# Optimization experiments

Measured on AMD Instinct MI355X. Metric: run time of the kernel, lower is better.

## Reference

```python
import jax, jax.numpy as jnp
import numpy as np

H, N, CH = 256, 64, 1

def _r2c(x):
    return x[..., 0] + 1j * x[..., 1]

def setup_inputs() -> dict:
    key = jax.random.key(0)
    kA, kB, kC, kdt = jax.random.split(key, 4)
    # Build a Hurwitz A (skew-Hermitian - 0.5*I) so dA = (I-dt/2 A)^-1 (I+dt/2 A) has spectral radius < 1
    M = jax.random.normal(kA, (H, N, N, 2), dtype=jnp.float32) / np.float32(np.sqrt(N))
    Mc = _r2c(M)
    Ac = 0.5 * (Mc - jnp.conjugate(jnp.swapaxes(Mc, -1, -2))) - 0.5 * jnp.eye(N, dtype=Mc.dtype)
    A = jnp.stack([Ac.real, Ac.imag], axis=-1)  # (H,N,N,2)
    B = jax.random.normal(kB, (H, N, 2), dtype=jnp.float32)
    C = jax.random.normal(kC, (CH, H, N, 2), dtype=jnp.float32)
    # log_dt uniform in [log(1e-3), log(1e-1)], shape (H,1) per bilinear docstring
    log_dt = jax.random.uniform(kdt, (H, 1), dtype=jnp.float32,
                                minval=np.float32(np.log(1e-3)), maxval=np.float32(np.log(1e-1)))
    return {"A": A, "B": B, "C": C, "log_dt": log_dt, "L": 2048}

def _bilinear(dt, Ac, Bc):
    # dt: (H,1), Ac: (H,N,N) complex, Bc: (H,N) complex
    n = Ac.shape[-1]
    I = jnp.eye(n, dtype=Ac.dtype)
    half = (dt.astype(Ac.real.dtype) / 2)[:, None]  # (H,1,1)
    A_back = I - half * Ac
    A_fwd = I + half * Ac
    dB = dt.astype(Ac.dtype) * jnp.linalg.solve(A_back, Bc[..., None])[..., 0]  # (H,N)
    dA = jnp.linalg.solve(A_back, A_fwd)  # (H,N,N)
    return dA, dB

def _krylov(L, dA, dB):
    # x[..., l] = dA^l dB via squaring-doubling, matches S4 krylov math
    x = dB[..., None]  # (H,N,1)
    A_ = dA
    while x.shape[-1] < L:
        x = jnp.concatenate([x, jnp.einsum('hnm,hml->hnl', A_, x)], axis=-1)
        A_ = A_ @ A_
    return x[..., :L]

def reference(A, B, C, log_dt, L):
    Ac, Bc, Cc = _r2c(A), _r2c(B), _r2c(C)
    dt = jnp.exp(log_dt)  # (H,1)
    dA, dB = _bilinear(dt, Ac, Bc)
    x = _krylov(L, dA, dB)  # (H,N,L) complex
    # k[c,h,l] = sum_n C[c,h,n] * (dA^l dB)[h,n]; torch .float() on complex keeps real part
    k = jnp.einsum('chn,hnl->chl', Cc, x).real.astype(jnp.float32)
    return k
```

## Files before the change

### kernel.cpp

```cpp
#include <hip/hip_runtime.h>
#include <math.h>

#define NH   256
#define NN   64
#define LSEQ 2048
#define RS   72
#define PSZ  4608
#define GSZ  2304
#define NTH  1024

typedef __attribute__((ext_vector_type(8))) short short8;
typedef __attribute__((ext_vector_type(4))) float float4_t;
typedef __attribute__((ext_vector_type(16))) float float16_t;
typedef unsigned short u16;

#define MFMA(a,b,c)   __builtin_amdgcn_mfma_f32_16x16x32_bf16((a),(b),(c),0,0,0)
#define MFMA32(a,b,c) __builtin_amdgcn_mfma_f32_32x32x16_bf16((a),(b),(c),0,0,0)
#define PERM_HI 0x07060302u

static __device__ __forceinline__ void split2(float v, unsigned& hb, unsigned& lb) {
    hb = __float_as_uint(v) & 0xffff0000u;
    lb = __float_as_uint(v - __uint_as_float(hb));
}
static __device__ __forceinline__ float ld2(const u16* hp, const u16* lp, int idx) {
    return __uint_as_float((unsigned)hp[idx] << 16)
         + __uint_as_float((unsigned)lp[idx] << 16);
}
static __device__ __forceinline__ short8 neg8(short8 v) {
    union { short8 s; int i[4]; } u; u.s = v;
#pragma unroll
    for (int m = 0; m < 4; ++m) u.i[m] ^= 0x80008000;
    return u.s;
}

static __device__ __forceinline__ void frag_vals(const unsigned* e, short8& hi, short8& lo) {
    unsigned lb[8];
#pragma unroll
    for (int m = 0; m < 8; ++m) {
        unsigned hv = e[m] & 0xffff0000u;
        lb[m] = __float_as_uint(__uint_as_float(e[m]) - __uint_as_float(hv));
    }
    union { short8 s; unsigned u[4]; } H, L;
#pragma unroll
    for (int m = 0; m < 4; ++m) {
        H.u[m] = __builtin_amdgcn_perm(e[2*m+1],  e[2*m],  PERM_HI);
        L.u[m] = __builtin_amdgcn_perm(lb[2*m+1], lb[2*m], PERM_HI);
    }
    hi = H.s; lo = L.s;
}

template<int ASZ, int BSZ, bool IMAG>
static __device__ __forceinline__ void cmm_tile(
    const u16* __restrict__ Ab, const u16* __restrict__ Bb,
    int arow, int bcol, int fq,
    float4_t& accP, float4_t& accN, float4_t& accI1, float4_t& accI2)
{
#pragma unroll
    for (int ks = 0; ks < 2; ++ks) {
        const int k0 = ks*32 + fq*8;
        const u16* ap = Ab + arow*RS + k0;
        const u16* bp = Bb + bcol*RS + k0;
        short8 Arh = *(const short8*)(ap);
        short8 Arl = *(const short8*)(ap + ASZ);
        short8 Aih = *(const short8*)(ap + 2*ASZ);
        short8 Ail = *(const short8*)(ap + 3*ASZ);
        short8 Brh = *(const short8*)(bp);
        short8 Brl = *(const short8*)(bp + BSZ);
        short8 Bih = *(const short8*)(bp + 2*BSZ);
        short8 Bil = *(const short8*)(bp + 3*BSZ);
        accP = MFMA(Arh, Brh, accP); accP = MFMA(Arh, Brl, accP); accP = MFMA(Arl, Brh, accP);
        accN = MFMA(Aih, Bih, accN); accN = MFMA(Aih, Bil, accN); accN = MFMA(Ail, Bih, accN);
        if (IMAG) {
            accI1 = MFMA(Arh, Bih, accI1); accI1 = MFMA(Arh, Bil, accI1); accI1 = MFMA(Arl, Bih, accI1);
            accI2 = MFMA(Aih, Brh, accI2); accI2 = MFMA(Aih, Brl, accI2); accI2 = MFMA(Ail, Brh, accI2);
        }
    }
}

template<int ASZ, int BSZ>
static __device__ __forceinline__ void cmm_pair(
    const u16* __restrict__ Ab, const u16* __restrict__ Bb,
    int arow, int bcol0, int fq,
    float4_t& P0, float4_t& N0, float4_t& I10, float4_t& I20,
    float4_t& P1, float4_t& N1, float4_t& I11, float4_t& I21)
{
#pragma unroll
    for (int ks = 0; ks < 2; ++ks) {
        const int k0 = ks*32 + fq*8;
        const u16* ap = Ab + arow*RS + k0;
        short8 Arh = *(const short8*)(ap);
        short8 Arl = *(const short8*)(ap + ASZ);
        short8 Aih = *(const short8*)(ap + 2*ASZ);
        short8 Ail = *(const short8*)(ap + 3*ASZ);
        {
            const u16* bp0 = Bb + bcol0*RS + k0;
            short8 Brh = *(const short8*)(bp0);
            short8 Brl = *(const short8*)(bp0 + BSZ);
            short8 Bih = *(const short8*)(bp0 + 2*BSZ);
            short8 Bil = *(const short8*)(bp0 + 3*BSZ);
            P0 = MFMA(Arh, Brh, P0); P0 = MFMA(Arh, Brl, P0); P0 = MFMA(Arl, Brh, P0);
            N0 = MFMA(Aih, Bih, N0); N0 = MFMA(Aih, Bil, N0); N0 = MFMA(Ail, Bih, N0);
            I10 = MFMA(Arh, Bih, I10); I10 = MFMA(Arh, Bil, I10); I10 = MFMA(Arl, Bih, I10);
            I20 = MFMA(Aih, Brh, I20); I20 = MFMA(Aih, Brl, I20); I20 = MFMA(Ail, Brh, I20);
        }
        {
            const u16* bp1 = Bb + (bcol0 + 16)*RS + k0;
            short8 Brh = *(const short8*)(bp1);
            short8 Brl = *(const short8*)(bp1 + BSZ);
            short8 Bih = *(const short8*)(bp1 + 2*BSZ);
            short8 Bil = *(const short8*)(bp1 + 3*BSZ);
            P1 = MFMA(Arh, Brh, P1); P1 = MFMA(Arh, Brl, P1); P1 = MFMA(Arl, Brh, P1);
            N1 = MFMA(Aih, Bih, N1); N1 = MFMA(Aih, Bil, N1); N1 = MFMA(Ail, Bih, N1);
            I11 = MFMA(Arh, Bih, I11); I11 = MFMA(Arh, Bil, I11); I11 = MFMA(Arl, Bih, I11);
            I21 = MFMA(Aih, Brh, I21); I21 = MFMA(Aih, Brl, I21); I21 = MFMA(Ail, Brh, I21);
        }
    }
}

template<int ASZ, int BSZ>
static __device__ __forceinline__ void cmm32_tile2(
    const u16* __restrict__ Ab, const u16* __restrict__ Bb,
    int arow, int bcol, int khalf,
    float16_t& R, float16_t& I)
{
#pragma unroll
    for (int ks = 0; ks < 4; ++ks) {
        const int k0 = ks*16 + khalf;
        const u16* ap = Ab + arow*RS + k0;
        const u16* bp = Bb + bcol*RS + k0;
        short8 Arh = *(const short8*)(ap);
        short8 Arl = *(const short8*)(ap + ASZ);
        short8 Aih = *(const short8*)(ap + 2*ASZ);
        short8 Ail = *(const short8*)(ap + 3*ASZ);
        short8 Brh = *(const short8*)(bp);
        short8 Brl = *(const short8*)(bp + BSZ);
        short8 Bih = *(const short8*)(bp + 2*BSZ);
        short8 Bil = *(const short8*)(bp + 3*BSZ);
        short8 nAih = neg8(Aih), nAil = neg8(Ail);
        R = MFMA32(Arh, Brh, R);  I = MFMA32(Arh, Bih, I);
        R = MFMA32(Arh, Brl, R);  I = MFMA32(Arh, Bil, I);
        R = MFMA32(Arl, Brh, R);  I = MFMA32(Arl, Bih, I);
        R = MFMA32(nAih, Bih, R); I = MFMA32(Aih, Brh, I);
        R = MFMA32(nAih, Bil, R); I = MFMA32(Aih, Brl, I);
        R = MFMA32(nAil, Bih, R); I = MFMA32(Ail, Brh, I);
    }
}

static __device__ __forceinline__ void store_P_vals(
    u16* XR, u16* XT, int ti, int bcol, int fq,
    const float* p_r, const float* p_i)
{
    unsigned hR[4], lR[4], hI[4], lI[4];
#pragma unroll
    for (int r = 0; r < 4; ++r) {
        split2(p_r[r], hR[r], lR[r]);
        split2(p_i[r], hI[r], lI[r]);
        int row = ti*16 + fq*4 + r;
        XR[row*RS + bcol]         = (u16)(hR[r] >> 16);
        XR[PSZ + row*RS + bcol]   = (u16)(lR[r] >> 16);
        XR[2*PSZ + row*RS + bcol] = (u16)(hI[r] >> 16);
        XR[3*PSZ + row*RS + bcol] = (u16)(lI[r] >> 16);
    }
    int tb = bcol*RS + ti*16 + fq*4;
    uint2 w;
    w.x = __builtin_amdgcn_perm(hR[1], hR[0], PERM_HI);
    w.y = __builtin_amdgcn_perm(hR[3], hR[2], PERM_HI);
    *(uint2*)&XT[tb] = w;
    w.x = __builtin_amdgcn_perm(lR[1], lR[0], PERM_HI);
    w.y = __builtin_amdgcn_perm(lR[3], lR[2], PERM_HI);
    *(uint2*)&XT[PSZ + tb] = w;
    w.x = __builtin_amdgcn_perm(hI[1], hI[0], PERM_HI);
    w.y = __builtin_amdgcn_perm(hI[3], hI[2], PERM_HI);
    *(uint2*)&XT[2*PSZ + tb] = w;
    w.x = __builtin_amdgcn_perm(lI[1], lI[0], PERM_HI);
    w.y = __builtin_amdgcn_perm(lI[3], lI[2], PERM_HI);
    *(uint2*)&XT[3*PSZ + tb] = w;
}

static __device__ __forceinline__ void store_P_vals32(
    u16* XR, u16* XT, int trow, int tcol, int lane,
    const float16_t& vR, const float16_t& vI)
{
    const int col = tcol + (lane & 31);
    const int hi4 = (lane >> 5) * 4;
#pragma unroll
    for (int q = 0; q < 4; ++q) {
        unsigned hR[4], lR[4], hI[4], lI[4];
#pragma unroll
        for (int rr = 0; rr < 4; ++rr) {
            const int g = 4*q + rr;
            split2(vR[g], hR[rr], lR[rr]);
            split2(vI[g], hI[rr], lI[rr]);
            const int row = trow + rr + 8*q + hi4;
            XR[row*RS + col]         = (u16)(hR[rr] >> 16);
            XR[PSZ + row*RS + col]   = (u16)(lR[rr] >> 16);
            XR[2*PSZ + row*RS + col] = (u16)(hI[rr] >> 16);
            XR[3*PSZ + row*RS + col] = (u16)(lI[rr] >> 16);
        }
        const int tb = col*RS + trow + 8*q + hi4;
        uint2 w;
        w.x = __builtin_amdgcn_perm(hR[1], hR[0], PERM_HI);
        w.y = __builtin_amdgcn_perm(hR[3], hR[2], PERM_HI);
        *(uint2*)&XT[tb] = w;
        w.x = __builtin_amdgcn_perm(lR[1], lR[0], PERM_HI);
        w.y = __builtin_amdgcn_perm(lR[3], lR[2], PERM_HI);
        *(uint2*)&XT[PSZ + tb] = w;
        w.x = __builtin_amdgcn_perm(hI[1], hI[0], PERM_HI);
        w.y = __builtin_amdgcn_perm(hI[3], hI[2], PERM_HI);
        *(uint2*)&XT[2*PSZ + tb] = w;
        w.x = __builtin_amdgcn_perm(lI[1], lI[0], PERM_HI);
        w.y = __builtin_amdgcn_perm(lI[3], lI[2], PERM_HI);
        *(uint2*)&XT[3*PSZ + tb] = w;
    }
}

__global__ __launch_bounds__(NTH, 4) void ssm_kernel(
    const float* __restrict__ Ag,
    const float* __restrict__ Bg,
    const float* __restrict__ Cg,
    const float* __restrict__ LogDt,
    float* __restrict__ outp)
{
    __shared__ __align__(16) unsigned char lds[130048];
    u16* XR = (u16*)(lds);
    u16* XT = (u16*)(lds +  36864);
    u16* XF = (u16*)(lds +  73728);
    u16* Gm = (u16*)(lds + 110592);
    float* bvr = (float*)(lds + 129024);
    float* bvi = (float*)(lds + 129280);
    float* urr = (float*)(lds + 129536);
    float* uri = (float*)(lds + 129792);

    const int t    = threadIdx.x;
    const int lane = t & 63;
    const int wv   = t >> 6;
    const int fm   = lane & 15, fq = lane >> 4;
    const int h    = blockIdx.x;

    const int tip  = wv >> 1, tjp = wv & 1;
    const int parow = tip*16 + fm;
    const int pb0   = tjp*32 + fm;
    const int pb1   = pb0 + 16;

    const int ti2 = (wv >> 1) & 1, tj2 = wv & 1;
    const int arow32 = ti2*32 + (lane & 31);
    const int bcol32 = tj2*32 + (lane & 31);
    const int khalf  = (lane >> 5) * 8;

    const float dt  = expf(LogDt[h]);
    const float hdt = 0.5f * dt;

    const float2* A2 = (const float2*)(Ag + (size_t)h * NN * NN * 2);
    const float4_t z4 = {0.f, 0.f, 0.f, 0.f};

#pragma unroll
    for (int e = 0; e < 4; ++e) {
        int idx = t + e*NTH;
        int i = idx >> 6, j = idx & 63;
        float2 a = A2[idx];
        unsigned hb, lb;
        split2((i == j ? 1.0f : 0.0f) + hdt * a.x, hb, lb);
        XR[i*RS + j]       = (u16)(hb >> 16);
        XR[PSZ + i*RS + j] = (u16)(lb >> 16);
        XT[j*RS + i]       = (u16)(hb >> 16);
        XT[PSZ + j*RS + i] = (u16)(lb >> 16);
        split2(hdt * a.y, hb, lb);
        XR[2*PSZ + i*RS + j] = (u16)(hb >> 16);
        XR[3*PSZ + i*RS + j] = (u16)(lb >> 16);
        XT[2*PSZ + j*RS + i] = (u16)(hb >> 16);
        XT[3*PSZ + j*RS + i] = (u16)(lb >> 16);
    }
    if (t < NN) {
        float2 bv = ((const float2*)Bg)[h*NN + t];
        float2 cv = ((const float2*)Cg)[h*NN + t];
        bvr[t] = bv.x; bvi[t] = bv.y;
        unsigned hb, lb;
        split2(cv.x, hb, lb);
        Gm[t]       = (u16)(hb >> 16);
        Gm[GSZ + t] = (u16)(lb >> 16);
        split2(cv.y, hb, lb);
        Gm[2*GSZ + t] = (u16)(hb >> 16);
        Gm[3*GSZ + t] = (u16)(lb >> 16);
    }
    __syncthreads();

    if (wv < 8) {
        float4_t P0 = z4, N0 = z4, I10 = z4, I20 = z4;
        float4_t P1 = z4, N1 = z4, I11 = z4, I21 = z4;
#pragma unroll
        for (int ks = 0; ks < 2; ++ks) {
            const int k0 = ks*32 + fq*8;
            unsigned vr[8], vi[8];
#pragma unroll
            for (int j = 0; j < 8; ++j) {
                float2 a = A2[parow*NN + k0 + j];
                vr[j] = __float_as_uint((parow == k0 + j ? 1.0f : 0.0f) - hdt * a.x);
                vi[j] = __float_as_uint(-hdt * a.y);
            }
            short8 Arh, Arl, Aih, Ail;
            frag_vals(vr, Arh, Arl);
            frag_vals(vi, Aih, Ail);
#pragma unroll
            for (int p = 0; p < 2; ++p) {
                const u16* bp = XT + (pb0 + p*16)*RS + k0;
                short8 Brh = *(const short8*)(bp);
                short8 Brl = *(const short8*)(bp + PSZ);
                short8 Bih = *(const short8*)(bp + 2*PSZ);
                short8 Bil = *(const short8*)(bp + 3*PSZ);
                float4_t &aP = p ? P1 : P0, &aN = p ? N1 : N0;
                float4_t &aI1 = p ? I11 : I10, &aI2 = p ? I21 : I20;
                aP = MFMA(Arh, Brh, aP); aP = MFMA(Arh, Brl, aP); aP = MFMA(Arl, Brh, aP);
                aN = MFMA(Aih, Bih, aN); aN = MFMA(Aih, Bil, aN); aN = MFMA(Ail, Bih, aN);
                aI1 = MFMA(Arh, Bih, aI1); aI1 = MFMA(Arh, Bil, aI1); aI1 = MFMA(Arl, Bih, aI1);
                aI2 = MFMA(Aih, Brh, aI2); aI2 = MFMA(Aih, Brl, aI2); aI2 = MFMA(Ail, Brh, aI2);
            }
        }
#pragma unroll
        for (int p = 0; p < 2; ++p) {
            const int bcol = pb0 + p*16;
            const float4_t &aP = p ? P1 : P0, &aN = p ? N1 : N0;
            const float4_t &aI1 = p ? I11 : I10, &aI2 = p ? I21 : I20;
#pragma unroll
            for (int rp = 0; rp < 2; ++rp) {
                int row0 = tip*16 + fq*4 + rp*2;
                unsigned h0, l0, h1, l1;
                split2(aP[rp*2]   - aN[rp*2],   h0, l0);
                split2(aP[rp*2+1] - aN[rp*2+1], h1, l1);
                *(unsigned*)&XF[bcol*RS + row0]       = __builtin_amdgcn_perm(h1, h0, PERM_HI);
                *(unsigned*)&XF[PSZ + bcol*RS + row0] = __builtin_amdgcn_perm(l1, l0, PERM_HI);
                split2(aI1[rp*2]   + aI2[rp*2],   h0, l0);
                split2(aI1[rp*2+1] + aI2[rp*2+1], h1, l1);
                *(unsigned*)&XF[2*PSZ + bcol*RS + row0] = __builtin_amdgcn_perm(h1, h0, PERM_HI);
                *(unsigned*)&XF[3*PSZ + bcol*RS + row0] = __builtin_amdgcn_perm(l1, l0, PERM_HI);
            }
        }
    }
    __syncthreads();

    {
        float4_t P0 = z4, N0 = z4, I10 = z4, I20 = z4;
        float4_t P1 = z4, N1 = z4, I11 = z4, I21 = z4;
        if (wv < 8)
            cmm_pair<PSZ, PSZ>(XR, XF, parow, pb0, fq, P0, N0, I10, I20, P1, N1, I11, I21);
        __syncthreads();
        if (wv < 8) {
#pragma unroll
            for (int p = 0; p < 2; ++p) {
                const int bcol = pb0 + p*16;
                const float4_t &aP = p ? P1 : P0, &aN = p ? N1 : N0;
                const float4_t &aI1 = p ? I11 : I10, &aI2 = p ? I21 : I20;
#pragma unroll
                for (int r = 0; r < 4; ++r) {
                    int row = tip*16 + fq*4 + r;
                    unsigned hb, lb;
                    split2(aP[r] - aN[r], hb, lb);
                    XR[row*RS + bcol]       = (u16)(hb >> 16);
                    XR[PSZ + row*RS + bcol] = (u16)(lb >> 16);
                    split2(aI1[r] + aI2[r], hb, lb);
                    XR[2*PSZ + row*RS + bcol] = (u16)(hb >> 16);
                    XR[3*PSZ + row*RS + bcol] = (u16)(lb >> 16);
                }
            }
        }
    }
    __syncthreads();

    {
        float p_r[2][4], p_i[2][4];
        if (wv < 8) {
            float4_t P0 = z4, N0 = z4, I10 = z4, I20 = z4;
            float4_t P1 = z4, N1 = z4, I11 = z4, I21 = z4;
            cmm_pair<PSZ, PSZ>(XR, XF, parow, pb0, fq, P0, N0, I10, I20, P1, N1, I11, I21);
#pragma unroll
            for (int p = 0; p < 2; ++p) {
                const int bcol = pb0 + p*16;
                const float4_t &aP = p ? P1 : P0, &aN = p ? N1 : N0;
                const float4_t &aI1 = p ? I11 : I10, &aI2 = p ? I21 : I20;
#pragma unroll
                for (int r = 0; r < 4; ++r) {
                    int row = tip*16 + fq*4 + r;
                    float2 a = A2[row*NN + bcol];
                    float dd  = (row == bcol ? 1.0f : 0.0f);
                    float x1r = dd + hdt * a.x;
                    float x1i = hdt * a.y;
                    float vvr = ld2(XR, XR + PSZ, row*RS + bcol);
                    float vvi = ld2(XR + 2*PSZ, XR + 3*PSZ, row*RS + bcol);
                    p_r[p][r] = 2.0f*(3.0f*x1r - 3.0f*vvr + (aP[r] - aN[r])) - dd;
                    p_i[p][r] = 2.0f*(3.0f*x1i - 3.0f*vvi + (aI1[r] + aI2[r]));
                }
            }
        }
        __syncthreads();
        if (wv < 8) {
            store_P_vals(XR, XT, tip, pb0, fq, p_r[0], p_i[0]);
            store_P_vals(XR, XT, tip, pb1, fq, p_r[1], p_i[1]);
        }
    }
    __syncthreads();

    {
        int n = t >> 4, part = t & 15;
        float ar = 0.f, ai = 0.f;
#pragma unroll
        for (int qq = 0; qq < 4; ++qq) {
            int k = part + 16*qq;
            float mr = ld2(XR, XR + PSZ, n*RS + k);
            float mi = ld2(XR + 2*PSZ, XR + 3*PSZ, n*RS + k);
            ar += mr*bvr[k] - mi*bvi[k];
            ai += mr*bvi[k] + mi*bvr[k];
        }
#pragma unroll
        for (int off = 8; off; off >>= 1) { ar += __shfl_xor(ar, off); ai += __shfl_xor(ai, off); }
        if (part == 0) { urr[n] = ar; uri[n] = ai; }
    }
    __syncthreads();

#pragma unroll 1
    for (int s = 1; s <= 9; ++s) {
        float16_t sR, sI;
        if (wv >= 8) {
            if (s == 1) {
                int n = (t >> 3) & 63, part = t & 7;
                float ar = 0.f, ai = 0.f;
#pragma unroll
                for (int qq = 0; qq < 8; ++qq) {
                    int k = part + 8*qq;
                    float mr = ld2(XR, XR + PSZ, n*RS + k);
                    float mi = ld2(XR + 2*PSZ, XR + 3*PSZ, n*RS + k);
                    ar += mr*urr[k] - mi*uri[k];
                    ai += mr*uri[k] + mi*urr[k];
                }
#pragma unroll
                for (int off = 4; off; off >>= 1) { ar += __shfl_xor(ar, off); ai += __shfl_xor(ai, off); }
                if (part == 0) {
                    float u_r = urr[n], u_i = uri[n];
                    unsigned hb, lb;
                    split2(hdt*(u_r + bvr[n]), hb, lb);
                    XF[n]       = (u16)(hb >> 16); XF[PSZ + n]       = (u16)(lb >> 16);
                    split2(hdt*(u_i + bvi[n]), hb, lb);
                    XF[2*PSZ + n] = (u16)(hb >> 16); XF[3*PSZ + n]   = (u16)(lb >> 16);
                    split2(hdt*(ar + u_r), hb, lb);
                    XF[RS + n]       = (u16)(hb >> 16); XF[PSZ + RS + n]   = (u16)(lb >> 16);
                    split2(hdt*(ai + u_i), hb, lb);
                    XF[2*PSZ + RS + n] = (u16)(hb >> 16); XF[3*PSZ + RS + n] = (u16)(lb >> 16);
                }
            } else if (s <= 6) {
                const int C = 1 << (s-1);
                const int w = wv - 8;
                const int nT = (s == 6) ? 8 : 4;
                if (w < nT) {
                    const int rt = w >> 2, ct = w & 3;
                    float4_t aP = z4, aN = z4, aI1 = z4, aI2 = z4;
                    cmm_tile<PSZ, PSZ, true>(XF, XR, rt*16 + fm, ct*16 + fm, fq, aP, aN, aI1, aI2);
#pragma unroll
                    for (int r = 0; r < 4; ++r) {
                        int orow = C + rt*16 + fq*4 + r;
                        int oc   = ct*16 + fm;
                        unsigned hb, lb;
                        split2(aP[r] - aN[r], hb, lb);
                        XF[orow*RS + oc]       = (u16)(hb >> 16);
                        XF[PSZ + orow*RS + oc] = (u16)(lb >> 16);
                        split2(aI1[r] + aI2[r], hb, lb);
                        XF[2*PSZ + orow*RS + oc] = (u16)(hb >> 16);
                        XF[3*PSZ + orow*RS + oc] = (u16)(lb >> 16);
                    }
                }
            } else {
                const int C = 1 << (s-7);
                const int w = wv - 8;
                if (w < 4) {
                    float4_t aP = z4, aN = z4, aI1 = z4, aI2 = z4;
                    cmm_tile<GSZ, PSZ, true>(Gm, XT, fm, w*16 + fm, fq, aP, aN, aI1, aI2);
#pragma unroll
                    for (int r = 0; r < 4; ++r) {
                        int orow = C + fq*4 + r;
                        int oc   = w*16 + fm;
                        unsigned hb, lb;
                        split2(aP[r] - aN[r], hb, lb);
                        Gm[orow*RS + oc]       = (u16)(hb >> 16);
                        Gm[GSZ + orow*RS + oc] = (u16)(lb >> 16);
                        split2(aI1[r] + aI2[r], hb, lb);
                        Gm[2*GSZ + orow*RS + oc] = (u16)(hb >> 16);
                        Gm[3*GSZ + orow*RS + oc] = (u16)(lb >> 16);
                    }
                }
            }
        } else if (wv < 4) {
#pragma unroll
            for (int g = 0; g < 16; ++g) { sR[g] = 0.f; sI[g] = 0.f; }
            cmm32_tile2<PSZ, PSZ>(XR, XT, arow32, bcol32, khalf, sR, sI);
        }
        __syncthreads();
        if (wv < 4) {
            store_P_vals32(XR, XT, ti2*32, tj2*32, lane, sR, sI);
        }
        __syncthreads();
    }

#pragma unroll 1
    for (int tt = 0; tt < 4; ++tt) {
        if (tt < 3 && wv < 4) {
            const int ab = tt * 8;
            float4_t aP = z4, aN = z4, aI1 = z4, aI2 = z4;
            cmm_tile<GSZ, PSZ, true>(Gm, XT, ab + fm, wv*16 + fm, fq, aP, aN, aI1, aI2);
#pragma unroll
            for (int r = 0; r < 4; ++r) {
                int orow = 8 + ab + fq*4 + r;
                if (orow < 32) {
                    int oc = wv*16 + fm;
                    unsigned hb, lb;
                    split2(aP[r] - aN[r], hb, lb);
                    Gm[orow*RS + oc]       = (u16)(hb >> 16);
                    Gm[GSZ + orow*RS + oc] = (u16)(lb >> 16);
                    split2(aI1[r] + aI2[r], hb, lb);
                    Gm[2*GSZ + orow*RS + oc] = (u16)(hb >> 16);
                    Gm[3*GSZ + orow*RS + oc] = (u16)(lb >> 16);
                }
            }
        }
        if (wv >= 4 && wv < 8) {
            const int jb = tt * 8;
            int ga = jb + fm; if (ga > 31) ga = 31;
            float4_t aP = z4, aN = z4, aI1 = z4, aI2 = z4;
            cmm_tile<GSZ, PSZ, false>(Gm, XF, ga, (wv-4)*16 + fm, fq, aP, aN, aI1, aI2);
            if (fq < 2) {
                size_t base = (size_t)h * LSEQ;
#pragma unroll
                for (int r = 0; r < 4; ++r)
                    outp[base + (jb + fq*4 + r)*NN + (wv-4)*16 + fm] = aP[r] - aN[r];
            }
        }
        if (tt < 3) __syncthreads();
    }
}

extern "C" void kernel_launch(void* const* d_in, const int* in_sizes, int n_in,
                              void* d_out, int out_size, void* d_ws, size_t ws_size,
                              hipStream_t stream) {
    const float* A  = (const float*)d_in[0];
    const float* B  = (const float*)d_in[1];
    const float* C  = (const float*)d_in[2];
    const float* ld = (const float*)d_in[3];
    float* out = (float*)d_out;
    ssm_kernel<<<dim3(NH), dim3(NTH), 0, stream>>>(A, B, C, ld, out);
}
```

Baseline: 95.16 us.

## Pack hi/lo bf16 split of XR matrix into single 32-bit LDS words

Replaces the four separate bf16 planes (real-hi, real-lo, imag-hi, imag-lo) of the XR matrix with two interleaved uint32 arrays holding hi and lo halves together, with a narrower row stride. Stores become one 32-bit write per value instead of two 16-bit writes, and fragment loads become two vector loads followed by perm unpacking. This aims to cut LDS store and load instruction counts and bank pressure. It also raises wave priority around two MFMA sections with s_setprio. The cost is extra perm instructions when unpacking fragments.

```diff
diff --git a/kernel.cpp b/kernel.cpp
--- a/kernel.cpp
+++ b/kernel.cpp
@@ -5,7 +5,9 @@
 #define NN   64
 #define LSEQ 2048
 #define RS   72
+#define RSW  68
 #define PSZ  4608
+#define PSZW 4352
 #define GSZ  2304
 #define NTH  1024
 
@@ -17,20 +19,37 @@
 #define MFMA(a,b,c)   __builtin_amdgcn_mfma_f32_16x16x32_bf16((a),(b),(c),0,0,0)
 #define MFMA32(a,b,c) __builtin_amdgcn_mfma_f32_32x32x16_bf16((a),(b),(c),0,0,0)
 #define PERM_HI 0x07060302u
+#define PERM_LO 0x05040100u
 
 static __device__ __forceinline__ void split2(float v, unsigned& hb, unsigned& lb) {
     hb = __float_as_uint(v) & 0xffff0000u;
     lb = __float_as_uint(v - __uint_as_float(hb));
 }
-static __device__ __forceinline__ float ld2(const u16* hp, const u16* lp, int idx) {
-    return __uint_as_float((unsigned)hp[idx] << 16)
-         + __uint_as_float((unsigned)lp[idx] << 16);
+static __device__ __forceinline__ unsigned pack2(float v) {
+    unsigned hb, lb; split2(v, hb, lb);
+    return __builtin_amdgcn_perm(hb, lb, PERM_HI);
+}
+static __device__ __forceinline__ float unpack2(unsigned w) {
+    return __uint_as_float(w & 0xffff0000u) + __uint_as_float(w << 16);
 }
 static __device__ __forceinline__ short8 neg8(short8 v) {
     union { short8 s; int i[4]; } u; u.s = v;
 #pragma unroll
     for (int m = 0; m < 4; ++m) u.i[m] ^= 0x80008000;
     return u.s;
+}
+
+static __device__ __forceinline__ void frag_packed(const unsigned* p, short8& hi, short8& lo) {
+    const uint4* q = (const uint4*)p;
+    uint4 d0 = q[0], d1 = q[1];
+    unsigned e[8] = {d0.x, d0.y, d0.z, d0.w, d1.x, d1.y, d1.z, d1.w};
+    union { short8 s; unsigned u[4]; } H, L;
+#pragma unroll
+    for (int m = 0; m < 4; ++m) {
+        H.u[m] = __builtin_amdgcn_perm(e[2*m+1], e[2*m], PERM_HI);
+        L.u[m] = __builtin_amdgcn_perm(e[2*m+1], e[2*m], PERM_LO);
+    }
+    hi = H.s; lo = L.s;
 }
 
 static __device__ __forceinline__ void frag_vals(const unsigned* e, short8& hi, short8& lo) {
@@ -50,7 +69,7 @@
 }
 
 template<int ASZ, int BSZ, bool IMAG>
-static __device__ __forceinline__ void cmm_tile(
+static __device__ __forceinline__ void cmm_ss(
     const u16* __restrict__ Ab, const u16* __restrict__ Bb,
     int arow, int bcol, int fq,
     float4_t& accP, float4_t& accN, float4_t& accI1, float4_t& accI2)
@@ -77,12 +96,12 @@
     }
 }
 
-template<int ASZ, int BSZ>
-static __device__ __forceinline__ void cmm_pair(
-    const u16* __restrict__ Ab, const u16* __restrict__ Bb,
-    int arow, int bcol0, int fq,
-    float4_t& P0, float4_t& N0, float4_t& I10, float4_t& I20,
-    float4_t& P1, float4_t& N1, float4_t& I11, float4_t& I21)
+template<int ASZ>
+static __device__ __forceinline__ void cmm_spk(
+    const u16* __restrict__ Ab, const unsigned* __restrict__ Bprl,
+    const unsigned* __restrict__ BpiI,
+    int arow, int bcol, int fq,
+    float4_t& accP, float4_t& accN, float4_t& accI1, float4_t& accI2)
 {
 #pragma unroll
     for (int ks = 0; ks < 2; ++ks) {
@@ -92,6 +111,30 @@
         short8 Arl = *(const short8*)(ap + ASZ);
         short8 Aih = *(const short8*)(ap + 2*ASZ);
         short8 Ail = *(const short8*)(ap + 3*ASZ);
+        short8 Brh, Brl, Bih, Bil;
+        frag_packed(Bprl + bcol*RSW + k0, Brh, Brl);
+        frag_packed(BpiI + bcol*RSW + k0, Bih, Bil);
+        accP = MFMA(Arh, Brh, accP); accP = MFMA(Arh, Brl, accP); accP = MFMA(Arl, Brh, accP);
+        accN = MFMA(Aih, Bih, accN); accN = MFMA(Aih, Bil, accN); accN = MFMA(Ail, Bih, accN);
+        accI1 = MFMA(Arh, Bih, accI1); accI1 = MFMA(Arh, Bil, accI1); accI1 = MFMA(Arl, Bih, accI1);
+        accI2 = MFMA(Aih, Brh, accI2); accI2 = MFMA(Aih, Brl, accI2); accI2 = MFMA(Ail, Brh, accI2);
+    }
+}
+
+template<int BSZ>
+static __device__ __forceinline__ void cmm_pair_pk(
+    const unsigned* __restrict__ Aprl, const unsigned* __restrict__ ApiI,
+    const u16* __restrict__ Bb,
+    int arow, int bcol0, int fq,
+    float4_t& P0, float4_t& N0, float4_t& I10, float4_t& I20,
+    float4_t& P1, float4_t& N1, float4_t& I11, float4_t& I21)
+{
+#pragma unroll
+    for (int ks = 0; ks < 2; ++ks) {
+        const int k0 = ks*32 + fq*8;
+        short8 Arh, Arl, Aih, Ail;
+        frag_packed(Aprl + arow*RSW + k0, Arh, Arl);
+        frag_packed(ApiI + arow*RSW + k0, Aih, Ail);
         {
             const u16* bp0 = Bb + bcol0*RS + k0;
             short8 Brh = *(const short8*)(bp0);
@@ -117,21 +160,20 @@
     }
 }
 
-template<int ASZ, int BSZ>
-static __device__ __forceinline__ void cmm32_tile2(
-    const u16* __restrict__ Ab, const u16* __restrict__ Bb,
+template<int BSZ>
+static __device__ __forceinline__ void cmm32_pk(
+    const unsigned* __restrict__ Aprl, const unsigned* __restrict__ ApiI,
+    const u16* __restrict__ Bb,
     int arow, int bcol, int khalf,
     float16_t& R, float16_t& I)
 {
 #pragma unroll
     for (int ks = 0; ks < 4; ++ks) {
         const int k0 = ks*16 + khalf;
-        const u16* ap = Ab + arow*RS + k0;
+        short8 Arh, Arl, Aih, Ail;
+        frag_packed(Aprl + arow*RSW + k0, Arh, Arl);
+        frag_packed(ApiI + arow*RSW + k0, Aih, Ail);
         const u16* bp = Bb + bcol*RS + k0;
-        short8 Arh = *(const short8*)(ap);
-        short8 Arl = *(const short8*)(ap + ASZ);
-        short8 Aih = *(const short8*)(ap + 2*ASZ);
-        short8 Ail = *(const short8*)(ap + 3*ASZ);
         short8 Brh = *(const short8*)(bp);
         short8 Brl = *(const short8*)(bp + BSZ);
         short8 Bih = *(const short8*)(bp + 2*BSZ);
@@ -146,22 +188,13 @@
     }
 }
 
-static __device__ __forceinline__ void store_P_vals(
-    u16* XR, u16* XT, int ti, int bcol, int fq,
-    const float* p_r, const float* p_i)
+static __device__ __forceinline__ void store_XT16(
+    u16* XT, int rowbase, int bcol, const float* p_r, const float* p_i)
 {
     unsigned hR[4], lR[4], hI[4], lI[4];
 #pragma unroll
-    for (int r = 0; r < 4; ++r) {
-        split2(p_r[r], hR[r], lR[r]);
-        split2(p_i[r], hI[r], lI[r]);
-        int row = ti*16 + fq*4 + r;
-        XR[row*RS + bcol]         = (u16)(hR[r] >> 16);
-        XR[PSZ + row*RS + bcol]   = (u16)(lR[r] >> 16);
-        XR[2*PSZ + row*RS + bcol] = (u16)(hI[r] >> 16);
-        XR[3*PSZ + row*RS + bcol] = (u16)(lI[r] >> 16);
-    }
-    int tb = bcol*RS + ti*16 + fq*4;
+    for (int r = 0; r < 4; ++r) { split2(p_r[r], hR[r], lR[r]); split2(p_i[r], hI[r], lI[r]); }
+    int tb = bcol*RS + rowbase;
     uint2 w;
     w.x = __builtin_amdgcn_perm(hR[1], hR[0], PERM_HI);
     w.y = __builtin_amdgcn_perm(hR[3], hR[2], PERM_HI);
@@ -177,43 +210,6 @@
     *(uint2*)&XT[3*PSZ + tb] = w;
 }
 
-static __device__ __forceinline__ void store_P_vals32(
-    u16* XR, u16* XT, int trow, int tcol, int lane,
-    const float16_t& vR, const float16_t& vI)
-{
-    const int col = tcol + (lane & 31);
-    const int hi4 = (lane >> 5) * 4;
-#pragma unroll
-    for (int q = 0; q < 4; ++q) {
-        unsigned hR[4], lR[4], hI[4], lI[4];
-#pragma unroll
-        for (int rr = 0; rr < 4; ++rr) {
-            const int g = 4*q + rr;
-            split2(vR[g], hR[rr], lR[rr]);
-            split2(vI[g], hI[rr], lI[rr]);
-            const int row = trow + rr + 8*q + hi4;
-            XR[row*RS + col]         = (u16)(hR[rr] >> 16);
-            XR[PSZ + row*RS + col]   = (u16)(lR[rr] >> 16);
-            XR[2*PSZ + row*RS + col] = (u16)(hI[rr] >> 16);
-            XR[3*PSZ + row*RS + col] = (u16)(lI[rr] >> 16);
-        }
-        const int tb = col*RS + trow + 8*q + hi4;
-        uint2 w;
-        w.x = __builtin_amdgcn_perm(hR[1], hR[0], PERM_HI);
-        w.y = __builtin_amdgcn_perm(hR[3], hR[2], PERM_HI);
-        *(uint2*)&XT[tb] = w;
-        w.x = __builtin_amdgcn_perm(lR[1], lR[0], PERM_HI);
-        w.y = __builtin_amdgcn_perm(lR[3], lR[2], PERM_HI);
-        *(uint2*)&XT[PSZ + tb] = w;
-        w.x = __builtin_amdgcn_perm(hI[1], hI[0], PERM_HI);
-        w.y = __builtin_amdgcn_perm(hI[3], hI[2], PERM_HI);
-        *(uint2*)&XT[2*PSZ + tb] = w;
-        w.x = __builtin_amdgcn_perm(lI[1], lI[0], PERM_HI);
-        w.y = __builtin_amdgcn_perm(lI[3], lI[2], PERM_HI);
-        *(uint2*)&XT[3*PSZ + tb] = w;
-    }
-}
-
 __global__ __launch_bounds__(NTH, 4) void ssm_kernel(
     const float* __restrict__ Ag,
     const float* __restrict__ Bg,
@@ -222,7 +218,8 @@
     float* __restrict__ outp)
 {
     __shared__ __align__(16) unsigned char lds[130048];
-    u16* XR = (u16*)(lds);
+    unsigned* XRrl = (unsigned*)(lds);
+    unsigned* XRiI = (unsigned*)(lds + 17408);
     u16* XT = (u16*)(lds +  36864);
     u16* XF = (u16*)(lds +  73728);
     u16* Gm = (u16*)(lds + 110592);
@@ -258,15 +255,15 @@
         int idx = t + e*NTH;
         int i = idx >> 6, j = idx & 63;
         float2 a = A2[idx];
+        float x1r = (i == j ? 1.0f : 0.0f) + hdt * a.x;
+        float x1i = hdt * a.y;
+        XRrl[i*RSW + j] = pack2(x1r);
+        XRiI[i*RSW + j] = pack2(x1i);
         unsigned hb, lb;
-        split2((i == j ? 1.0f : 0.0f) + hdt * a.x, hb, lb);
-        XR[i*RS + j]       = (u16)(hb >> 16);
-        XR[PSZ + i*RS + j] = (u16)(lb >> 16);
+        split2(x1r, hb, lb);
         XT[j*RS + i]       = (u16)(hb >> 16);
         XT[PSZ + j*RS + i] = (u16)(lb >> 16);
-        split2(hdt * a.y, hb, lb);
-        XR[2*PSZ + i*RS + j] = (u16)(hb >> 16);
-        XR[3*PSZ + i*RS + j] = (u16)(lb >> 16);
+        split2(x1i, hb, lb);
         XT[2*PSZ + j*RS + i] = (u16)(hb >> 16);
         XT[3*PSZ + j*RS + i] = (u16)(lb >> 16);
     }
@@ -341,24 +338,19 @@
         float4_t P0 = z4, N0 = z4, I10 = z4, I20 = z4;
         float4_t P1 = z4, N1 = z4, I11 = z4, I21 = z4;
         if (wv < 8)
-            cmm_pair<PSZ, PSZ>(XR, XF, parow, pb0, fq, P0, N0, I10, I20, P1, N1, I11, I21);
+            cmm_pair_pk<PSZ>(XRrl, XRiI, XF, parow, pb0, fq, P0, N0, I10, I20, P1, N1, I11, I21);
         __syncthreads();
         if (wv < 8) {
 #pragma unroll
             for (int p = 0; p < 2; ++p) {
                 const int bcol = pb0 + p*16;
-                const float4_t &aP = p ? P1 : P0, &aN = p ? N1 : N0;
-                const float4_t &aI1 = p ? I11 : I10, &aI2 = p ? I21 : I20;
 #pragma unroll
                 for (int r = 0; r < 4; ++r) {
                     int row = tip*16 + fq*4 + r;
-                    unsigned hb, lb;
-                    split2(aP[r] - aN[r], hb, lb);
-                    XR[row*RS + bcol]       = (u16)(hb >> 16);
-                    XR[PSZ + row*RS + bcol] = (u16)(lb >> 16);
-                    split2(aI1[r] + aI2[r], hb, lb);
-                    XR[2*PSZ + row*RS + bcol] = (u16)(hb >> 16);
-                    XR[3*PSZ + row*RS + bcol] = (u16)(lb >> 16);
+                    float vr = (p ? P1[r] : P0[r]) - (p ? N1[r] : N0[r]);
+                    float vi = (p ? I11[r] : I10[r]) + (p ? I21[r] : I20[r]);
+                    XRrl[row*RSW + bcol] = pack2(vr);
+                    XRiI[row*RSW + bcol] = pack2(vi);
                 }
             }
         }
@@ -370,7 +362,7 @@
         if (wv < 8) {
             float4_t P0 = z4, N0 = z4, I10 = z4, I20 = z4;
             float4_t P1 = z4, N1 = z4, I11 = z4, I21 = z4;
-            cmm_pair<PSZ, PSZ>(XR, XF, parow, pb0, fq, P0, N0, I10, I20, P1, N1, I11, I21);
+            cmm_pair_pk<PSZ>(XRrl, XRiI, XF, parow, pb0, fq, P0, N0, I10, I20, P1, N1, I11, I21);
 #pragma unroll
             for (int p = 0; p < 2; ++p) {
                 const int bcol = pb0 + p*16;
@@ -383,8 +375,8 @@
                     float dd  = (row == bcol ? 1.0f : 0.0f);
                     float x1r = dd + hdt * a.x;
                     float x1i = hdt * a.y;
-                    float vvr = ld2(XR, XR + PSZ, row*RS + bcol);
-                    float vvi = ld2(XR + 2*PSZ, XR + 3*PSZ, row*RS + bcol);
+                    float vvr = unpack2(XRrl[row*RSW + bcol]);
+                    float vvi = unpack2(XRiI[row*RSW + bcol]);
                     p_r[p][r] = 2.0f*(3.0f*x1r - 3.0f*vvr + (aP[r] - aN[r])) - dd;
                     p_i[p][r] = 2.0f*(3.0f*x1i - 3.0f*vvi + (aI1[r] + aI2[r]));
                 }
@@ -392,20 +384,33 @@
         }
         __syncthreads();
         if (wv < 8) {
-            store_P_vals(XR, XT, tip, pb0, fq, p_r[0], p_i[0]);
-            store_P_vals(XR, XT, tip, pb1, fq, p_r[1], p_i[1]);
+#pragma unroll
+            for (int p = 0; p < 2; ++p) {
+                const int bcol = pb0 + p*16;
+#pragma unroll
+                for (int r = 0; r < 4; ++r) {
+                    int row = tip*16 + fq*4 + r;
+                    XRrl[row*RSW + bcol] = pack2(p_r[p][r]);
+                    XRiI[row*RSW + bcol] = pack2(p_i[p][r]);
+                }
+                store_XT16(XT, tip*16 + fq*4, bcol, p_r[p], p_i[p]);
+            }
         }
     }
     __syncthreads();
 
     {
         int n = t >> 4, part = t & 15;
+        uint4 Wr = *(const uint4*)(XRrl + n*RSW + part*4);
+        uint4 Wi = *(const uint4*)(XRiI + n*RSW + part*4);
+        unsigned wr[4] = {Wr.x, Wr.y, Wr.z, Wr.w};
+        unsigned wi[4] = {Wi.x, Wi.y, Wi.z, Wi.w};
         float ar = 0.f, ai = 0.f;
 #pragma unroll
-        for (int qq = 0; qq < 4; ++qq) {
-            int k = part + 16*qq;
-            float mr = ld2(XR, XR + PSZ, n*RS + k);
-            float mi = ld2(XR + 2*PSZ, XR + 3*PSZ, n*RS + k);
+        for (int e = 0; e < 4; ++e) {
+            float mr = unpack2(wr[e]);
+            float mi = unpack2(wi[e]);
+            int k = part*4 + e;
             ar += mr*bvr[k] - mi*bvi[k];
             ai += mr*bvi[k] + mi*bvr[k];
         }
@@ -421,12 +426,18 @@
         if (wv >= 8) {
             if (s == 1) {
                 int n = (t >> 3) & 63, part = t & 7;
+                const unsigned* rp0 = XRrl + n*RSW + part*8;
+                const unsigned* ip0 = XRiI + n*RSW + part*8;
+                uint4 Wr0 = *(const uint4*)(rp0), Wr1 = *(const uint4*)(rp0 + 4);
+                uint4 Wi0 = *(const uint4*)(ip0), Wi1 = *(const uint4*)(ip0 + 4);
+                unsigned wr[8] = {Wr0.x, Wr0.y, Wr0.z, Wr0.w, Wr1.x, Wr1.y, Wr1.z, Wr1.w};
+                unsigned wi[8] = {Wi0.x, Wi0.y, Wi0.z, Wi0.w, Wi1.x, Wi1.y, Wi1.z, Wi1.w};
                 float ar = 0.f, ai = 0.f;
 #pragma unroll
-                for (int qq = 0; qq < 8; ++qq) {
-                    int k = part + 8*qq;
-                    float mr = ld2(XR, XR + PSZ, n*RS + k);
-                    float mi = ld2(XR + 2*PSZ, XR + 3*PSZ, n*RS + k);
+                for (int e = 0; e < 8; ++e) {
+                    float mr = unpack2(wr[e]);
+                    float mi = unpack2(wi[e]);
+                    int k = part*8 + e;
                     ar += mr*urr[k] - mi*uri[k];
                     ai += mr*uri[k] + mi*urr[k];
                 }
@@ -451,7 +462,7 @@
                 if (w < nT) {
                     const int rt = w >> 2, ct = w & 3;
                     float4_t aP = z4, aN = z4, aI1 = z4, aI2 = z4;
-                    cmm_tile<PSZ, PSZ, true>(XF, XR, rt*16 + fm, ct*16 + fm, fq, aP, aN, aI1, aI2);
+                    cmm_spk<PSZ>(XF, XRrl, XRiI, rt*16 + fm, ct*16 + fm, fq, aP, aN, aI1, aI2);
 #pragma unroll
                     for (int r = 0; r < 4; ++r) {
                         int orow = C + rt*16 + fq*4 + r;
@@ -470,7 +481,7 @@
                 const int w = wv - 8;
                 if (w < 4) {
                     float4_t aP = z4, aN = z4, aI1 = z4, aI2 = z4;
-                    cmm_tile<GSZ, PSZ, true>(Gm, XT, fm, w*16 + fm, fq, aP, aN, aI1, aI2);
+                    cmm_ss<GSZ, PSZ, true>(Gm, XT, fm, w*16 + fm, fq, aP, aN, aI1, aI2);
 #pragma unroll
                     for (int r = 0; r < 4; ++r) {
                         int orow = C + fq*4 + r;
@@ -488,11 +499,27 @@
         } else if (wv < 4) {
 #pragma unroll
             for (int g = 0; g < 16; ++g) { sR[g] = 0.f; sI[g] = 0.f; }
-            cmm32_tile2<PSZ, PSZ>(XR, XT, arow32, bcol32, khalf, sR, sI);
+            __builtin_amdgcn_s_setprio(1);
+            cmm32_pk<PSZ>(XRrl, XRiI, XT, arow32, bcol32, khalf, sR, sI);
+            __builtin_amdgcn_s_setprio(0);
         }
         __syncthreads();
         if (wv < 4) {
-            store_P_vals32(XR, XT, ti2*32, tj2*32, lane, sR, sI);
+            const int col = tj2*32 + (lane & 31);
+            const int hi4 = (lane >> 5) * 4;
+#pragma unroll
+            for (int q = 0; q < 4; ++q) {
+                float r4[4], i4[4];
+#pragma unroll
+                for (int rr = 0; rr < 4; ++rr) { r4[rr] = sR[4*q+rr]; i4[rr] = sI[4*q+rr]; }
+                const int rowb = ti2*32 + 8*q + hi4;
+#pragma unroll
+                for (int rr = 0; rr < 4; ++rr) {
+                    XRrl[(rowb + rr)*RSW + col] = pack2(r4[rr]);
+                    XRiI[(rowb + rr)*RSW + col] = pack2(i4[rr]);
+                }
+                store_XT16(XT, rowb, col, r4, i4);
+            }
         }
         __syncthreads();
     }
@@ -502,7 +529,7 @@
         if (tt < 3 && wv < 4) {
             const int ab = tt * 8;
             float4_t aP = z4, aN = z4, aI1 = z4, aI2 = z4;
-            cmm_tile<GSZ, PSZ, true>(Gm, XT, ab + fm, wv*16 + fm, fq, aP, aN, aI1, aI2);
+            cmm_ss<GSZ, PSZ, true>(Gm, XT, ab + fm, wv*16 + fm, fq, aP, aN, aI1, aI2);
 #pragma unroll
             for (int r = 0; r < 4; ++r) {
                 int orow = 8 + ab + fq*4 + r;
@@ -522,7 +549,9 @@
             const int jb = tt * 8;
             int ga = jb + fm; if (ga > 31) ga = 31;
             float4_t aP = z4, aN = z4, aI1 = z4, aI2 = z4;
-            cmm_tile<GSZ, PSZ, false>(Gm, XF, ga, (wv-4)*16 + fm, fq, aP, aN, aI1, aI2);
+            __builtin_amdgcn_s_setprio(1);
+            cmm_ss<GSZ, PSZ, false>(Gm, XF, ga, (wv-4)*16 + fm, fq, aP, aN, aI1, aI2);
+            __builtin_amdgcn_s_setprio(0);
             if (fq < 2) {
                 size_t base = (size_t)h * LSEQ;
 #pragma unroll
```

New measurement: 93.35 us. Within noise of the previous version (-1.9%).
